# Kernel tuning notes

Measured on AMD Instinct MI355X. Metric: run time of the kernel, lower is better.

The kernel has to match this reference:

```python
import jax, jax.numpy as jnp
import numpy as np

N, E, D, D_NODE, D_EDGE, T, L = 100000, 640000, 128, 128, 32, 8, 3
EPS = 1e-5


def _layernorm(x, g, b):
    m = jnp.mean(x, -1, keepdims=True)
    v = jnp.mean((x - m) ** 2, -1, keepdims=True)
    return (x - m) * jax.lax.rsqrt(v + EPS) * g + b


def setup_inputs() -> dict:
    key = jax.random.key(0)
    ks = jax.random.split(key, 24)
    s = 0.02
    inp = {
        "x": jax.random.normal(ks[0], (N, D_NODE), jnp.float32),
        "edge_index": jax.random.randint(ks[1], (2, E), 0, N, jnp.int64),
        "edge_attr": jax.random.normal(ks[2], (E, D_EDGE), jnp.float32),
        "node_w": jax.random.normal(ks[3], (D_NODE, D), jnp.float32) * s,
        "node_b": jnp.zeros((D,), jnp.float32),
        "edge_w": jax.random.normal(ks[4], (D_EDGE, D), jnp.float32) * s,
        "edge_b": jnp.zeros((D,), jnp.float32),
        "msg_w1": jax.random.normal(ks[5], (L, D, D), jnp.float32) * s,
        "msg_b1": jnp.zeros((L, D), jnp.float32),
        "msg_w2": jax.random.normal(ks[6], (L, D, D), jnp.float32) * s,
        "msg_b2": jnp.zeros((L, D), jnp.float32),
        "upd_w1": jax.random.normal(ks[7], (L, D, 2 * D), jnp.float32) * s,
        "upd_b1": jnp.zeros((L, 2 * D), jnp.float32),
        "upd_w2": jax.random.normal(ks[8], (L, 2 * D, D), jnp.float32) * s,
        "upd_b2": jnp.zeros((L, D), jnp.float32),
        "ln_g": jnp.ones((L, D), jnp.float32),
        "ln_b": jnp.zeros((L, D), jnp.float32),
        "out_g": jnp.ones((D,), jnp.float32),
        "out_b": jnp.zeros((D,), jnp.float32),
    }
    return inp


def _pool_seg_ids():
    seg = T - 1
    cs = -(-N // seg)  # torch.chunk uses ceil chunk size
    sizes = []
    rem = N
    while rem > 0:
        sizes.append(min(cs, rem))
        rem -= cs
    return np.repeat(np.arange(len(sizes)), sizes), np.asarray(sizes, np.float32)


_SEG_IDS_NP, _SEG_SIZES_NP = _pool_seg_ids()


def reference(x, edge_index, edge_attr, node_w, node_b, edge_w, edge_b,
              msg_w1, msg_b1, msg_w2, msg_b2, upd_w1, upd_b1, upd_w2, upd_b2,
              ln_g, ln_b, out_g, out_b):
    node = x @ node_w + node_b                     # [N, D]
    edge_emb = edge_attr @ edge_w + edge_b         # [E, D]
    src, dst = edge_index[0], edge_index[1]
    deg = jax.ops.segment_sum(jnp.ones((E,), node.dtype), dst, num_segments=N)[:, None]
    deg = jnp.maximum(deg, 1.0)
    for i in range(L):
        h = jax.nn.gelu((node[src] + edge_emb) @ msg_w1[i] + msg_b1[i], approximate=False)
        msg = h @ msg_w2[i] + msg_b2[i]            # [E, D]
        agg = jax.ops.segment_sum(msg, dst, num_segments=N) / deg
        u = jax.nn.gelu(agg @ upd_w1[i] + upd_b1[i], approximate=False)
        u = u @ upd_w2[i] + upd_b2[i]
        node = _layernorm(node + u, ln_g[i], ln_b[i])
    # pooling: global mean token + (T-1) contiguous-segment means
    global_tok = node.mean(0, keepdims=True)       # [1, D]
    seg_ids = jnp.asarray(_SEG_IDS_NP)
    sums = jax.ops.segment_sum(node, seg_ids, num_segments=T - 1)
    seg_tok = sums / jnp.asarray(_SEG_SIZES_NP)[:, None]
    stacked = jnp.concatenate([global_tok, seg_tok], axis=0)  # [T, D]
    return _layernorm(stacked, out_g, out_b)
```

## Files before the change

### kernel.cpp

```cpp
#include <hip/hip_runtime.h>
#include <hip/hip_bf16.h>

#define N_NODES 100000
#define N_EDGES 640000
#define DD 128
#define DE 32
#define SCAN_B 256
#define SCAN_NB ((N_NODES + SCAN_B - 1) / SCAN_B)

typedef __attribute__((ext_vector_type(8))) short bf8v;
typedef __attribute__((ext_vector_type(4))) float f4v;

__device__ __forceinline__ float gelu_f(float x) {
    return 0.5f * x * (1.0f + erff(x * 0.70710678118654752f));
}
__device__ __forceinline__ float gelu_t(float x) {
    float y = 0.7978845608f * (x + 0.044715f * x * x * x);
    float t = __expf(-2.0f * fabsf(y));
    float th = (1.0f - t) / (1.0f + t);
    th = copysignf(th, y);
    return 0.5f * x * (1.0f + th);
}
__device__ __forceinline__ float bf2f(ushort u) {
    union { uint u; float f; } t; t.u = ((uint)u) << 16; return t.f;
}
__device__ __forceinline__ ushort f2bf(float f) {
    union { float f; uint u; } t; t.f = f;
    uint r = (t.u + 0x7fffu + ((t.u >> 16) & 1u)) >> 16;
    return (ushort)r;
}

__device__ __forceinline__ void stage_w(ushort* lwgt, const ushort* __restrict__ src,
                                        int stride, int w, int lane) {
#pragma unroll
    for (int k = 0; k < 8; k++) {
        int o = (w * 8192) + k * 1024 + lane * 16;
        int row = o >> 8;
        int swz = o ^ ((row & 7) << 4);
        const ushort* g = src + (size_t)row * stride + ((swz & 255) >> 1);
        __builtin_amdgcn_global_load_lds(
            (const __attribute__((address_space(1))) void*)g,
            (__attribute__((address_space(3))) void*)(lwgt + (w * 8192 + k * 1024) / 2),
            16, 0, 0);
    }
}

__device__ __forceinline__ void gemm_l(const bf8v* a, const ushort* lwgt,
                                       int cq, int quad, f4v* acc) {
    const char* lb = (const char*)lwgt;
    int sw = (cq & 7) << 4;
    __builtin_amdgcn_s_setprio(1);
#pragma unroll
    for (int ct = 0; ct < 8; ct++) {
#pragma unroll
        for (int kc = 0; kc < 4; kc++) {
            int addr = (((ct * 16 + cq) << 8) + (kc << 6) + (quad << 4)) ^ sw;
            acc[ct] = __builtin_amdgcn_mfma_f32_16x16x32_bf16(a[kc],
                *(const bf8v*)(lb + addr), acc[ct], 0, 0, 0);
        }
    }
    __builtin_amdgcn_s_setprio(0);
}

__global__ void k_count(const int* __restrict__ ei, int* __restrict__ cnt) {
    int e = blockIdx.x * blockDim.x + threadIdx.x;
    if (e < N_EDGES) atomicAdd(&cnt[ei[N_EDGES + e]], 1);
}

__global__ void k_scan1(const int* __restrict__ cnt, int* __restrict__ bsum) {
    __shared__ int s[SCAN_B];
    int i = blockIdx.x * SCAN_B + threadIdx.x;
    int v = (i < N_NODES) ? cnt[i] : 0;
    s[threadIdx.x] = v;
    __syncthreads();
    for (int off = SCAN_B / 2; off > 0; off >>= 1) {
        if (threadIdx.x < off) s[threadIdx.x] += s[threadIdx.x + off];
        __syncthreads();
    }
    if (threadIdx.x == 0) bsum[blockIdx.x] = s[0];
}

__global__ void k_scan2(int* __restrict__ bsum) {
    __shared__ int s[512];
    int t = threadIdx.x;
    int v = (t < SCAN_NB) ? bsum[t] : 0;
    s[t] = v;
    __syncthreads();
    for (int off = 1; off < 512; off <<= 1) {
        int u = (t >= off) ? s[t - off] : 0;
        __syncthreads();
        s[t] += u;
        __syncthreads();
    }
    if (t < SCAN_NB) bsum[t] = s[t] - v;
}

__global__ void k_scan3(const int* __restrict__ cnt, const int* __restrict__ bsum,
                        int* __restrict__ cursor, float* __restrict__ flag,
                        float* __restrict__ invdeg) {
    __shared__ int s[SCAN_B];
    int i = blockIdx.x * SCAN_B + threadIdx.x;
    int v = (i < N_NODES) ? cnt[i] : 0;
    s[threadIdx.x] = v;
    __syncthreads();
    for (int off = 1; off < SCAN_B; off <<= 1) {
        int u = (threadIdx.x >= off) ? s[threadIdx.x - off] : 0;
        __syncthreads();
        s[threadIdx.x] += u;
        __syncthreads();
    }
    if (i < N_NODES) {
        int excl = s[threadIdx.x] - v + bsum[blockIdx.x];
        cursor[i] = excl;
        flag[i] = (v > 0) ? 1.0f : 0.0f;
        invdeg[i] = (v > 0) ? 1.0f / (float)v : 0.0f;
    }
}

__global__ void k_scatter(const int* __restrict__ ei, int* __restrict__ cursor,
                          int* __restrict__ eord, int* __restrict__ esrc,
                          int* __restrict__ edst) {
    int e = blockIdx.x * blockDim.x + threadIdx.x;
    if (e < N_EDGES) {
        int d = ei[N_EDGES + e];
        int pos = atomicAdd(&cursor[d], 1);
        eord[pos] = e;
        esrc[pos] = ei[e];
        edst[pos] = d;
    }
}

__global__ void k_prep(const float* __restrict__ edge_w, const float* __restrict__ edge_b,
                       const float* __restrict__ msg_w1, const float* __restrict__ msg_b1,
                       ushort* __restrict__ WeT, float* __restrict__ bc) {
    int j = threadIdx.x;
    int c = blockIdx.x;
    int l = blockIdx.y;
    const float* w1 = msg_w1 + (size_t)l * DD * DD;
    if (c < DE) {
        float s = 0.0f;
        for (int k = 0; k < DD; k++) s += edge_w[c*DD + k] * w1[k*DD + j];
        WeT[((size_t)l*DD + j)*DE + c] = f2bf(s);
    } else {
        float s = msg_b1[l*DD + j];
        for (int k = 0; k < DD; k++) s += edge_b[k] * w1[k*DD + j];
        bc[l*DD + j] = s;
    }
}

struct TDesc { const float* src; ushort* dst; int R; int C; };
struct TPack { TDesc d[13]; };

__global__ void k_tball(TPack p) {
    TDesc t = p.d[blockIdx.y];
    int idx = blockIdx.x * 256 + threadIdx.x;
    if (idx < t.R * t.C) {
        int r = idx / t.C, c = idx % t.C;
        t.dst[(size_t)c * t.R + r] = f2bf(t.src[idx]);
    }
}

__global__ __launch_bounds__(256, 3) void k_embed(
    const float* __restrict__ x, const ushort* __restrict__ WT,
    const float* __restrict__ bias, const ushort* __restrict__ W1T,
    float* __restrict__ node, ushort* __restrict__ slotA, int M)
{
    __shared__ __align__(16) ushort lwgt[16384];
    __shared__ ushort tr[4][16 * 136];
    int tid = threadIdx.x, lane = tid & 63, w = tid >> 6;
    int base = (blockIdx.x * 4 + w) * 16;
    bool act = base < M;
    int cq = lane & 15, quad = lane >> 4;
    ushort* trw = tr[w];
    f4v acc[8];
    bf8v a[4];

    stage_w(lwgt, WT, DD, w, lane);
    if (act) {
        const float* Af = x + (size_t)(base + cq) * DD;
#pragma unroll
        for (int kc = 0; kc < 4; kc++) {
            float4 v0 = *(const float4*)(Af + kc * 32 + quad * 8);
            float4 v1 = *(const float4*)(Af + kc * 32 + quad * 8 + 4);
            bf8v t;
            t[0]=(short)f2bf(v0.x); t[1]=(short)f2bf(v0.y); t[2]=(short)f2bf(v0.z); t[3]=(short)f2bf(v0.w);
            t[4]=(short)f2bf(v1.x); t[5]=(short)f2bf(v1.y); t[6]=(short)f2bf(v1.z); t[7]=(short)f2bf(v1.w);
            a[kc] = t;
        }
    }
    __syncthreads();
    int r0 = base + quad * 4;
    bf8v a2[4];
    if (act) {
#pragma unroll
        for (int ct = 0; ct < 8; ct++) acc[ct] = 0.0f;
        gemm_l(a, lwgt, cq, quad, acc);
#pragma unroll
        for (int ct = 0; ct < 8; ct++) {
            int col = ct * 16 + cq;
            float b_ = bias[col];
#pragma unroll
            for (int i = 0; i < 4; i++) {
                float v = acc[ct][i] + b_;
                node[(size_t)(r0 + i) * DD + col] = v;
                trw[(quad * 4 + i) * 136 + col] = f2bf(v);
            }
        }
#pragma unroll
        for (int kc = 0; kc < 4; kc++)
            a2[kc] = *(const bf8v*)(trw + cq * 136 + kc * 32 + quad * 8);
    }
    __syncthreads();
    stage_w(lwgt, W1T, DD, w, lane);
    __syncthreads();
    if (act) {
#pragma unroll
        for (int ct = 0; ct < 8; ct++) acc[ct] = 0.0f;
        gemm_l(a2, lwgt, cq, quad, acc);
#pragma unroll
        for (int ct = 0; ct < 8; ct++) {
            int col = ct * 16 + cq;
#pragma unroll
            for (int i = 0; i < 4; i++)
                slotA[(size_t)(r0 + i) * DD + col] = f2bf(acc[ct][i]);
        }
    }
}

__global__ __launch_bounds__(256) void k_msg(
    const int* __restrict__ eord, const float* __restrict__ edge_attr,
    const ushort* __restrict__ WeT, const float* __restrict__ bcv,
    const int* __restrict__ esrc, const int* __restrict__ edst,
    const ushort* __restrict__ slotA, float* __restrict__ aggf)
{
    __shared__ ushort tr[4][16 * 136];
    __shared__ int2 sd[4][16];
    int tid = threadIdx.x, lane = tid & 63, w = tid >> 6;
    int jt = (blockIdx.x * 4 + w) * 16;
    int cq = lane & 15, quad = lane >> 4;
    ushort* trw = tr[w];

    if (lane < 16) {
        int2 v; v.x = esrc[jt + lane]; v.y = edst[jt + lane];
        sd[w][lane] = v;
    }
    {
        int e = eord[jt + cq];
        const float* ea = edge_attr + (size_t)e * DE + quad * 8;
        float4 v0 = *(const float4*)(ea);
        float4 v1 = *(const float4*)(ea + 4);
        bf8v a;
        a[0]=(short)f2bf(v0.x); a[1]=(short)f2bf(v0.y); a[2]=(short)f2bf(v0.z); a[3]=(short)f2bf(v0.w);
        a[4]=(short)f2bf(v1.x); a[5]=(short)f2bf(v1.y); a[6]=(short)f2bf(v1.z); a[7]=(short)f2bf(v1.w);
        __builtin_amdgcn_s_setprio(1);
#pragma unroll
        for (int ct = 0; ct < 8; ct++) {
            bf8v b = *(const bf8v*)(WeT + (size_t)(ct * 16 + cq) * DE + quad * 8);
            f4v z; z = 0.0f;
            f4v r = __builtin_amdgcn_mfma_f32_16x16x32_bf16(a, b, z, 0, 0, 0);
            int col = ct * 16 + cq;
            float b_ = bcv[col];
#pragma unroll
            for (int i = 0; i < 4; i++)
                trw[(quad * 4 + i) * 136 + col] = f2bf(r[i] + b_);
        }
        __builtin_amdgcn_s_setprio(0);
    }
    float a0 = 0.0f, a1 = 0.0f;
#pragma unroll
    for (int r = 0; r < 16; r++) {
        int2 s = sd[w][r];
        uint em = *(const uint*)(trw + r * 136 + 2 * lane);
        uint nw = *(const uint*)(slotA + (size_t)s.x * DD + 2 * lane);
        a0 += gelu_t(bf2f((ushort)(em & 0xffffu)) + bf2f((ushort)(nw & 0xffffu)));
        a1 += gelu_t(bf2f((ushort)(em >> 16)) + bf2f((ushort)(nw >> 16)));
        bool flush = (r == 15) || (sd[w][r + 1].y != s.y);
        if (flush) {
            float* p = aggf + (size_t)s.y * DD + 2 * lane;
            atomicAdd(p, a0);
            atomicAdd(p + 1, a1);
            a0 = 0.0f; a1 = 0.0f;
        }
    }
}

template<int ZERO>
__global__ void k_norm(const float* __restrict__ invdeg, float* __restrict__ aggf,
                       ushort* __restrict__ aggb) {
    int idx = blockIdx.x * 256 + threadIdx.x;
    int n = idx >> 5, c4 = (idx & 31) * 4;
    float inv = invdeg[n];
    float* p = aggf + (size_t)n * DD + c4;
    float4 v = *(const float4*)p;
    ushort4 o;
    o.x = f2bf(v.x * inv); o.y = f2bf(v.y * inv);
    o.z = f2bf(v.z * inv); o.w = f2bf(v.w * inv);
    *(ushort4*)(aggb + (size_t)n * DD + c4) = o;
    if (ZERO) *(float4*)p = float4{0.0f, 0.0f, 0.0f, 0.0f};
}

template<int FUSE>
__global__ __launch_bounds__(256, 3) void k_mlp(
    const ushort* __restrict__ agg,
    const ushort* __restrict__ w2T, const float* __restrict__ b2,
    const float* __restrict__ flag,
    const ushort* __restrict__ u1T, const float* __restrict__ bu1,
    const ushort* __restrict__ u2T, const float* __restrict__ bu2,
    float* __restrict__ node,
    const float* __restrict__ lg, const float* __restrict__ lb,
    const ushort* __restrict__ w1nT, ushort* __restrict__ slotA, int M)
{
    __shared__ __align__(16) ushort lwgt[16384];
    __shared__ ushort tr[4][16 * 136];
    int tid = threadIdx.x, lane = tid & 63, w = tid >> 6;
    int base = (blockIdx.x * 4 + w) * 16;
    bool act = base < M;
    int cq = lane & 15, quad = lane >> 4;
    ushort* trw = tr[w];
    f4v acc[8];
    bf8v a[4], a2[4];

    stage_w(lwgt, w2T, DD, w, lane);
    if (act) {
        const ushort* Ab = agg + (size_t)(base + cq) * DD;
#pragma unroll
        for (int kc = 0; kc < 4; kc++)
            a[kc] = *(const bf8v*)(Ab + kc * 32 + quad * 8);
    }
    __syncthreads();
    if (act) {
#pragma unroll
        for (int ct = 0; ct < 8; ct++) acc[ct] = 0.0f;
        gemm_l(a, lwgt, cq, quad, acc);
        float fl[4];
#pragma unroll
        for (int i = 0; i < 4; i++) fl[i] = flag[base + quad * 4 + i];
#pragma unroll
        for (int ct = 0; ct < 8; ct++) {
            int col = ct * 16 + cq;
            float b_ = b2[col];
#pragma unroll
            for (int i = 0; i < 4; i++)
                trw[(quad * 4 + i) * 136 + col] = f2bf(acc[ct][i] + fl[i] * b_);
        }
#pragma unroll
        for (int kc = 0; kc < 4; kc++)
            a2[kc] = *(const bf8v*)(trw + cq * 136 + kc * 32 + quad * 8);
    }

    f4v accU[8];
#pragma unroll
    for (int ct = 0; ct < 8; ct++) accU[ct] = 0.0f;
#pragma unroll
    for (int h = 0; h < 2; h++) {
        __syncthreads();
        stage_w(lwgt, u1T + (size_t)h * 128 * DD, DD, w, lane);
        __syncthreads();
        bf8v tf[4];
        if (act) {
#pragma unroll
            for (int ct = 0; ct < 8; ct++) acc[ct] = 0.0f;
            gemm_l(a2, lwgt, cq, quad, acc);
#pragma unroll
            for (int ct = 0; ct < 8; ct++) {
                int col = ct * 16 + cq;
                float b_ = bu1[h * 128 + col];
#pragma unroll
                for (int i = 0; i < 4; i++)
                    trw[(quad * 4 + i) * 136 + col] = f2bf(gelu_f(acc[ct][i] + b_));
            }
#pragma unroll
            for (int kc = 0; kc < 4; kc++)
                tf[kc] = *(const bf8v*)(trw + cq * 136 + kc * 32 + quad * 8);
        }
        __syncthreads();
        stage_w(lwgt, u2T + (size_t)h * 128, 256, w, lane);
        __syncthreads();
        if (act) gemm_l(tf, lwgt, cq, quad, accU);
    }

    int r0 = base + quad * 4;
    if (act) {
        float xv[8][4], lgc[8], lbc[8];
#pragma unroll
        for (int ct = 0; ct < 8; ct++) {
            int col = ct * 16 + cq;
            float b_ = bu2[col];
            lgc[ct] = lg[col]; lbc[ct] = lb[col];
#pragma unroll
            for (int i = 0; i < 4; i++)
                xv[ct][i] = accU[ct][i] + b_ + node[(size_t)(r0 + i) * DD + col];
        }
#pragma unroll
        for (int i = 0; i < 4; i++) {
            float s = 0.0f;
#pragma unroll
            for (int ct = 0; ct < 8; ct++) s += xv[ct][i];
            s += __shfl_xor(s, 1); s += __shfl_xor(s, 2);
            s += __shfl_xor(s, 4); s += __shfl_xor(s, 8);
            float m = s * (1.0f / 128.0f);
            float vv = 0.0f;
#pragma unroll
            for (int ct = 0; ct < 8; ct++) { float d = xv[ct][i] - m; vv += d * d; }
            vv += __shfl_xor(vv, 1); vv += __shfl_xor(vv, 2);
            vv += __shfl_xor(vv, 4); vv += __shfl_xor(vv, 8);
            float inv = rsqrtf(vv * (1.0f / 128.0f) + 1e-5f);
#pragma unroll
            for (int ct = 0; ct < 8; ct++) {
                int col = ct * 16 + cq;
                float y = (xv[ct][i] - m) * inv * lgc[ct] + lbc[ct];
                node[(size_t)(r0 + i) * DD + col] = y;
                if (FUSE) trw[(quad * 4 + i) * 136 + col] = f2bf(y);
            }
        }
    }

    if (FUSE) {
        __syncthreads();
        stage_w(lwgt, w1nT, DD, w, lane);
        __syncthreads();
        if (act) {
            bf8v nf[4];
#pragma unroll
            for (int kc = 0; kc < 4; kc++)
                nf[kc] = *(const bf8v*)(trw + cq * 136 + kc * 32 + quad * 8);
#pragma unroll
            for (int ct = 0; ct < 8; ct++) acc[ct] = 0.0f;
            gemm_l(nf, lwgt, cq, quad, acc);
#pragma unroll
            for (int ct = 0; ct < 8; ct++) {
                int col = ct * 16 + cq;
#pragma unroll
                for (int i = 0; i < 4; i++)
                    slotA[(size_t)(r0 + i) * DD + col] = f2bf(acc[ct][i]);
            }
        }
    }
}

__global__ void k_pool_partial(const float* __restrict__ node, float* __restrict__ partial) {
    int seg = blockIdx.x, chunk = blockIdx.y, j = threadIdx.x;
    int segbase = seg * 14286;
    int segcnt = (seg == 6) ? 14284 : 14286;
    const int per = 112;
    int lo = chunk * per, hi = min(lo + per, segcnt);
    float s = 0.0f;
    for (int r = lo; r < hi; r++) s += node[(size_t)(segbase + r) * DD + j];
    partial[(size_t)(seg * 128 + chunk) * DD + j] = s;
}

__global__ void k_pool_final(const float* __restrict__ partial, const float* __restrict__ g,
                             const float* __restrict__ b, float* __restrict__ out) {
    __shared__ float red[128];
    int j = threadIdx.x;
    float tok[8];
    float tot = 0.0f;
#pragma unroll
    for (int s = 0; s < 7; s++) {
        float v = 0.0f;
        for (int c = 0; c < 128; c++) v += partial[(size_t)(s * 128 + c) * DD + j];
        tok[1 + s] = v / ((s == 6) ? 14284.0f : 14286.0f);
        tot += v;
    }
    tok[0] = tot / 100000.0f;
    for (int t = 0; t < 8; t++) {
        float x = tok[t];
        red[j] = x; __syncthreads();
        for (int off = 64; off > 0; off >>= 1) {
            if (j < off) red[j] += red[j + off];
            __syncthreads();
        }
        float m = red[0] / 128.0f;
        __syncthreads();
        float d = x - m;
        red[j] = d * d; __syncthreads();
        for (int off = 64; off > 0; off >>= 1) {
            if (j < off) red[j] += red[j + off];
            __syncthreads();
        }
        float var = red[0] / 128.0f;
        __syncthreads();
        out[t * DD + j] = d * rsqrtf(var + 1e-5f) * g[j] + b[j];
    }
}

extern "C" void kernel_launch(void* const* d_in, const int* in_sizes, int n_in,
                              void* d_out, int out_size, void* d_ws, size_t ws_size,
                              hipStream_t stream) {
    const float* x         = (const float*)d_in[0];
    const int*   ei        = (const int*)d_in[1];
    const float* edge_attr = (const float*)d_in[2];
    const float* node_w    = (const float*)d_in[3];
    const float* node_b    = (const float*)d_in[4];
    const float* edge_w    = (const float*)d_in[5];
    const float* edge_b    = (const float*)d_in[6];
    const float* msg_w1    = (const float*)d_in[7];
    const float* msg_b1    = (const float*)d_in[8];
    const float* msg_w2    = (const float*)d_in[9];
    const float* msg_b2    = (const float*)d_in[10];
    const float* upd_w1    = (const float*)d_in[11];
    const float* upd_b1    = (const float*)d_in[12];
    const float* upd_w2    = (const float*)d_in[13];
    const float* upd_b2    = (const float*)d_in[14];
    const float* ln_g      = (const float*)d_in[15];
    const float* ln_b      = (const float*)d_in[16];
    const float* out_g     = (const float*)d_in[17];
    const float* out_b     = (const float*)d_in[18];
    float* out = (float*)d_out;

    char* pw = (char*)d_ws;
    auto alloc = [&](size_t bytes) -> void* {
        void* r = (void*)pw;
        pw += (bytes + 255) & ~(size_t)255;
        return r;
    };
    float*  node_f  = (float*) alloc((size_t)N_NODES * DD * 4);
    ushort* slotA   = (ushort*)alloc((size_t)N_NODES * DD * 2);
    ushort* aggb    = (ushort*)alloc((size_t)N_NODES * DD * 2);
    float*  aggf    = (float*) alloc((size_t)N_NODES * DD * 4);
    float*  bc      = (float*) alloc((size_t)3 * DD * 4);
    ushort* WeT     = (ushort*)alloc((size_t)3 * DD * DE * 2);
    float*  partial = (float*) alloc((size_t)7 * 128 * DD * 4);
    float*  degflag = (float*) alloc((size_t)N_NODES * 4);
    float*  invdeg  = (float*) alloc((size_t)N_NODES * 4);
    ushort* node_wT = (ushort*)alloc((size_t)DD * DD * 2);
    ushort* msg_w1T = (ushort*)alloc((size_t)3 * DD * DD * 2);
    ushort* msg_w2T = (ushort*)alloc((size_t)3 * DD * DD * 2);
    ushort* upd_w1T = (ushort*)alloc((size_t)3 * 256 * DD * 2);
    ushort* upd_w2T = (ushort*)alloc((size_t)3 * DD * 256 * 2);
    int* cnt        = (int*)   alloc((size_t)N_NODES * 4);
    int* cursor     = (int*)   alloc((size_t)N_NODES * 4);
    int* bsum       = (int*)   alloc((size_t)512 * 4);
    int* eord       = (int*)   alloc((size_t)N_EDGES * 4);
    int* esrc       = (int*)   alloc((size_t)N_EDGES * 4);
    int* edst       = (int*)   alloc((size_t)N_EDGES * 4);

    hipMemsetAsync(cnt, 0, N_NODES * sizeof(int), stream);
    hipMemsetAsync(aggf, 0, (size_t)N_NODES * DD * 4, stream);
    k_count  <<<(N_EDGES + 255) / 256, 256, 0, stream>>>(ei, cnt);
    k_scan1  <<<SCAN_NB, SCAN_B, 0, stream>>>(cnt, bsum);
    k_scan2  <<<1, 512, 0, stream>>>(bsum);
    k_scan3  <<<SCAN_NB, SCAN_B, 0, stream>>>(cnt, bsum, cursor, degflag, invdeg);
    k_scatter<<<(N_EDGES + 255) / 256, 256, 0, stream>>>(ei, cursor, eord, esrc, edst);
    k_prep   <<<dim3(DE + 1, 3), DD, 0, stream>>>(edge_w, edge_b, msg_w1, msg_b1, WeT, bc);

    TPack tp;
    tp.d[0] = { node_w, node_wT, DD, DD };
    for (int l = 0; l < 3; l++) {
        tp.d[1 + l*4 + 0] = { msg_w1 + (size_t)l*DD*DD,  msg_w1T + (size_t)l*DD*DD,  DD, DD };
        tp.d[1 + l*4 + 1] = { msg_w2 + (size_t)l*DD*DD,  msg_w2T + (size_t)l*DD*DD,  DD, DD };
        tp.d[1 + l*4 + 2] = { upd_w1 + (size_t)l*DD*256, upd_w1T + (size_t)l*256*DD, DD, 256 };
        tp.d[1 + l*4 + 3] = { upd_w2 + (size_t)l*256*DD, upd_w2T + (size_t)l*DD*256, 256, DD };
    }
    k_tball<<<dim3(128, 13), 256, 0, stream>>>(tp);

    const int GB = (N_NODES / 16 + 3) / 4;
    const int MSG_GB = N_EDGES / 64;
    const int NORM_GB = N_NODES * 32 / 256;
    k_embed<<<GB, 256, 0, stream>>>(x, node_wT, node_b, msg_w1T, node_f, slotA, N_NODES);

    for (int l = 0; l < 3; l++) {
        k_msg<<<MSG_GB, 256, 0, stream>>>(eord, edge_attr, WeT + (size_t)l*DD*DE,
            bc + (size_t)l*DD, esrc, edst, slotA, aggf);
        if (l < 2) {
            k_norm<1><<<NORM_GB, 256, 0, stream>>>(invdeg, aggf, aggb);
            k_mlp<1><<<GB, 256, 0, stream>>>(aggb,
                msg_w2T + (size_t)l*DD*DD, msg_b2 + (size_t)l*DD, degflag,
                upd_w1T + (size_t)l*256*DD, upd_b1 + (size_t)l*256,
                upd_w2T + (size_t)l*DD*256, upd_b2 + (size_t)l*DD,
                node_f, ln_g + (size_t)l*DD, ln_b + (size_t)l*DD,
                msg_w1T + (size_t)(l+1)*DD*DD, slotA, N_NODES);
        } else {
            k_norm<0><<<NORM_GB, 256, 0, stream>>>(invdeg, aggf, aggb);
            k_mlp<0><<<GB, 256, 0, stream>>>(aggb,
                msg_w2T + (size_t)l*DD*DD, msg_b2 + (size_t)l*DD, degflag,
                upd_w1T + (size_t)l*256*DD, upd_b1 + (size_t)l*256,
                upd_w2T + (size_t)l*DD*256, upd_b2 + (size_t)l*DD,
                node_f, ln_g + (size_t)l*DD, ln_b + (size_t)l*DD,
                msg_w1T, slotA, N_NODES);
        }
    }

    k_pool_partial<<<dim3(7, 128), DD, 0, stream>>>(node_f, partial);
    k_pool_final  <<<1, DD, 0, stream>>>(partial, out_g, out_b, out);
}
```

Measured before the change: 955.3 us.

## Pre-permute edge attributes to bf16, widen MLP blocks to eight waves, cheaper GELU

Adds a one-time kernel that gathers edge_attr into destination-sorted order as bf16, so each of the three message layers reads contiguous half-size rows instead of doing an indirect fp32 gather and conversion. The node MLP and embed kernels move to 512-thread blocks, so each block amortises its weight staging into shared memory over twice as many rows. The tanh-GELU approximation drops the abs/copysign/divide form for an exp plus hardware reciprocal. The costs are an extra buffer and kernel launch, a possible loss of occupancy with the larger blocks, and possible overflow in the exp for large inputs.

```diff
diff --git a/kernel.cpp b/kernel.cpp
--- a/kernel.cpp
+++ b/kernel.cpp
@@ -16,9 +16,8 @@
 }
 __device__ __forceinline__ float gelu_t(float x) {
     float y = 0.7978845608f * (x + 0.044715f * x * x * x);
-    float t = __expf(-2.0f * fabsf(y));
-    float th = (1.0f - t) / (1.0f + t);
-    th = copysignf(th, y);
+    float t = __expf(2.0f * y);
+    float th = 1.0f - 2.0f * __builtin_amdgcn_rcpf(t + 1.0f);
     return 0.5f * x * (1.0f + th);
 }
 __device__ __forceinline__ float bf2f(ushort u) {
@@ -30,17 +29,19 @@
     return (ushort)r;
 }
 
+template<int NW>
 __device__ __forceinline__ void stage_w(ushort* lwgt, const ushort* __restrict__ src,
                                         int stride, int w, int lane) {
-#pragma unroll
-    for (int k = 0; k < 8; k++) {
-        int o = (w * 8192) + k * 1024 + lane * 16;
+    constexpr int SEG = 32768 / NW;
+#pragma unroll
+    for (int k = 0; k < SEG / 1024; k++) {
+        int o = w * SEG + k * 1024 + lane * 16;
         int row = o >> 8;
         int swz = o ^ ((row & 7) << 4);
         const ushort* g = src + (size_t)row * stride + ((swz & 255) >> 1);
         __builtin_amdgcn_global_load_lds(
             (const __attribute__((address_space(1))) void*)g,
-            (__attribute__((address_space(3))) void*)(lwgt + (w * 8192 + k * 1024) / 2),
+            (__attribute__((address_space(3))) void*)(lwgt + (w * SEG + k * 1024) / 2),
             16, 0, 0);
     }
 }
@@ -128,6 +129,18 @@
         esrc[pos] = ei[e];
         edst[pos] = d;
     }
+}
+
+__global__ void k_eperm(const int* __restrict__ eord, const float* __restrict__ ea,
+                        ushort* __restrict__ eat) {
+    int slot = blockIdx.x * 32 + (threadIdx.x >> 3);
+    int l8 = threadIdx.x & 7;
+    int e = eord[slot];
+    const float* s = ea + (size_t)e * DE + l8 * 4;
+    float4 v = *(const float4*)s;
+    ushort4 o;
+    o.x = f2bf(v.x); o.y = f2bf(v.y); o.z = f2bf(v.z); o.w = f2bf(v.w);
+    *(ushort4*)(eat + (size_t)slot * DE + l8 * 4) = o;
 }
 
 __global__ void k_prep(const float* __restrict__ edge_w, const float* __restrict__ edge_b,
@@ -160,22 +173,22 @@
     }
 }
 
-__global__ __launch_bounds__(256, 3) void k_embed(
+__global__ __launch_bounds__(512, 4) void k_embed(
     const float* __restrict__ x, const ushort* __restrict__ WT,
     const float* __restrict__ bias, const ushort* __restrict__ W1T,
     float* __restrict__ node, ushort* __restrict__ slotA, int M)
 {
     __shared__ __align__(16) ushort lwgt[16384];
-    __shared__ ushort tr[4][16 * 136];
+    __shared__ ushort tr[8][16 * 136];
     int tid = threadIdx.x, lane = tid & 63, w = tid >> 6;
-    int base = (blockIdx.x * 4 + w) * 16;
+    int base = (blockIdx.x * 8 + w) * 16;
     bool act = base < M;
     int cq = lane & 15, quad = lane >> 4;
     ushort* trw = tr[w];
     f4v acc[8];
     bf8v a[4];
 
-    stage_w(lwgt, WT, DD, w, lane);
+    stage_w<8>(lwgt, WT, DD, w, lane);
     if (act) {
         const float* Af = x + (size_t)(base + cq) * DD;
 #pragma unroll
@@ -211,7 +224,7 @@
             a2[kc] = *(const bf8v*)(trw + cq * 136 + kc * 32 + quad * 8);
     }
     __syncthreads();
-    stage_w(lwgt, W1T, DD, w, lane);
+    stage_w<8>(lwgt, W1T, DD, w, lane);
     __syncthreads();
     if (act) {
 #pragma unroll
@@ -228,7 +241,7 @@
 }
 
 __global__ __launch_bounds__(256) void k_msg(
-    const int* __restrict__ eord, const float* __restrict__ edge_attr,
+    const ushort* __restrict__ eat,
     const ushort* __restrict__ WeT, const float* __restrict__ bcv,
     const int* __restrict__ esrc, const int* __restrict__ edst,
     const ushort* __restrict__ slotA, float* __restrict__ aggf)
@@ -245,13 +258,7 @@
         sd[w][lane] = v;
     }
     {
-        int e = eord[jt + cq];
-        const float* ea = edge_attr + (size_t)e * DE + quad * 8;
-        float4 v0 = *(const float4*)(ea);
-        float4 v1 = *(const float4*)(ea + 4);
-        bf8v a;
-        a[0]=(short)f2bf(v0.x); a[1]=(short)f2bf(v0.y); a[2]=(short)f2bf(v0.z); a[3]=(short)f2bf(v0.w);
-        a[4]=(short)f2bf(v1.x); a[5]=(short)f2bf(v1.y); a[6]=(short)f2bf(v1.z); a[7]=(short)f2bf(v1.w);
+        bf8v a = *(const bf8v*)(eat + (size_t)(jt + cq) * DE + quad * 8);
         __builtin_amdgcn_s_setprio(1);
 #pragma unroll
         for (int ct = 0; ct < 8; ct++) {
@@ -300,7 +307,7 @@
 }
 
 template<int FUSE>
-__global__ __launch_bounds__(256, 3) void k_mlp(
+__global__ __launch_bounds__(512, 4) void k_mlp(
     const ushort* __restrict__ agg,
     const ushort* __restrict__ w2T, const float* __restrict__ b2,
     const float* __restrict__ flag,
@@ -311,16 +318,16 @@
     const ushort* __restrict__ w1nT, ushort* __restrict__ slotA, int M)
 {
     __shared__ __align__(16) ushort lwgt[16384];
-    __shared__ ushort tr[4][16 * 136];
+    __shared__ ushort tr[8][16 * 136];
     int tid = threadIdx.x, lane = tid & 63, w = tid >> 6;
-    int base = (blockIdx.x * 4 + w) * 16;
+    int base = (blockIdx.x * 8 + w) * 16;
     bool act = base < M;
     int cq = lane & 15, quad = lane >> 4;
     ushort* trw = tr[w];
     f4v acc[8];
     bf8v a[4], a2[4];
 
-    stage_w(lwgt, w2T, DD, w, lane);
+    stage_w<8>(lwgt, w2T, DD, w, lane);
     if (act) {
         const ushort* Ab = agg + (size_t)(base + cq) * DD;
 #pragma unroll
@@ -354,7 +361,7 @@
 #pragma unroll
     for (int h = 0; h < 2; h++) {
         __syncthreads();
-        stage_w(lwgt, u1T + (size_t)h * 128 * DD, DD, w, lane);
+        stage_w<8>(lwgt, u1T + (size_t)h * 128 * DD, DD, w, lane);
         __syncthreads();
         bf8v tf[4];
         if (act) {
@@ -374,7 +381,7 @@
                 tf[kc] = *(const bf8v*)(trw + cq * 136 + kc * 32 + quad * 8);
         }
         __syncthreads();
-        stage_w(lwgt, u2T + (size_t)h * 128, 256, w, lane);
+        stage_w<8>(lwgt, u2T + (size_t)h * 128, 256, w, lane);
         __syncthreads();
         if (act) gemm_l(tf, lwgt, cq, quad, accU);
     }
@@ -417,7 +424,7 @@
 
     if (FUSE) {
         __syncthreads();
-        stage_w(lwgt, w1nT, DD, w, lane);
+        stage_w<8>(lwgt, w1nT, DD, w, lane);
         __syncthreads();
         if (act) {
             bf8v nf[4];
@@ -518,6 +525,7 @@
     ushort* slotA   = (ushort*)alloc((size_t)N_NODES * DD * 2);
     ushort* aggb    = (ushort*)alloc((size_t)N_NODES * DD * 2);
     float*  aggf    = (float*) alloc((size_t)N_NODES * DD * 4);
+    ushort* eat     = (ushort*)alloc((size_t)N_EDGES * DE * 2);
     float*  bc      = (float*) alloc((size_t)3 * DD * 4);
     ushort* WeT     = (ushort*)alloc((size_t)3 * DD * DE * 2);
     float*  partial = (float*) alloc((size_t)7 * 128 * DD * 4);
@@ -542,6 +550,7 @@
     k_scan2  <<<1, 512, 0, stream>>>(bsum);
     k_scan3  <<<SCAN_NB, SCAN_B, 0, stream>>>(cnt, bsum, cursor, degflag, invdeg);
     k_scatter<<<(N_EDGES + 255) / 256, 256, 0, stream>>>(ei, cursor, eord, esrc, edst);
+    k_eperm  <<<N_EDGES / 32, 256, 0, stream>>>(eord, edge_attr, eat);
     k_prep   <<<dim3(DE + 1, 3), DD, 0, stream>>>(edge_w, edge_b, msg_w1, msg_b1, WeT, bc);
 
     TPack tp;
@@ -554,17 +563,17 @@
     }
     k_tball<<<dim3(128, 13), 256, 0, stream>>>(tp);
 
-    const int GB = (N_NODES / 16 + 3) / 4;
+    const int GB = (N_NODES / 16 + 7) / 8;
     const int MSG_GB = N_EDGES / 64;
     const int NORM_GB = N_NODES * 32 / 256;
-    k_embed<<<GB, 256, 0, stream>>>(x, node_wT, node_b, msg_w1T, node_f, slotA, N_NODES);
+    k_embed<<<GB, 512, 0, stream>>>(x, node_wT, node_b, msg_w1T, node_f, slotA, N_NODES);
 
     for (int l = 0; l < 3; l++) {
-        k_msg<<<MSG_GB, 256, 0, stream>>>(eord, edge_attr, WeT + (size_t)l*DD*DE,
+        k_msg<<<MSG_GB, 256, 0, stream>>>(eat, WeT + (size_t)l*DD*DE,
             bc + (size_t)l*DD, esrc, edst, slotA, aggf);
         if (l < 2) {
             k_norm<1><<<NORM_GB, 256, 0, stream>>>(invdeg, aggf, aggb);
-            k_mlp<1><<<GB, 256, 0, stream>>>(aggb,
+            k_mlp<1><<<GB, 512, 0, stream>>>(aggb,
                 msg_w2T + (size_t)l*DD*DD, msg_b2 + (size_t)l*DD, degflag,
                 upd_w1T + (size_t)l*256*DD, upd_b1 + (size_t)l*256,
                 upd_w2T + (size_t)l*DD*256, upd_b2 + (size_t)l*DD,
@@ -572,7 +581,7 @@
                 msg_w1T + (size_t)(l+1)*DD*DD, slotA, N_NODES);
         } else {
             k_norm<0><<<NORM_GB, 256, 0, stream>>>(invdeg, aggf, aggb);
-            k_mlp<0><<<GB, 256, 0, stream>>>(aggb,
+            k_mlp<0><<<GB, 512, 0, stream>>>(aggb,
                 msg_w2T + (size_t)l*DD*DD, msg_b2 + (size_t)l*DD, degflag,
                 upd_w1T + (size_t)l*256*DD, upd_b1 + (size_t)l*256,
                 upd_w2T + (size_t)l*DD*256, upd_b2 + (size_t)l*DD,
```

New measurement: 1.035 ms. +8.3%, slower.
